# Kernel tuning notes

Hardware: AMD Instinct MI355X
Metric: run time of the kernel (lower is better)

Reference implementation:

```python
import jax, jax.numpy as jnp
import numpy as np

HEADS = 4
DIM_HEAD = 32


def setup_inputs() -> dict:
    key = jax.random.key(0)
    k1, k2, k3, k4 = jax.random.split(key, 4)
    dim = 64
    hidden = HEADS * DIM_HEAD  # 128
    x = jax.random.normal(k1, (1, dim, 16, 16, 16), jnp.float32)
    # Conv3d 1x1 kernels collapse to [out_ch, in_ch] matrices
    w_qkv = jax.random.normal(k2, (hidden * 3, dim), jnp.float32) * 0.05
    w_out = jax.random.normal(k3, (dim, hidden), jnp.float32) * 0.05
    b_out = jax.random.normal(k4, (dim,), jnp.float32) * 0.05
    return {"x": x, "w_qkv": w_qkv, "w_out": w_out, "b_out": b_out}


def reference(x, w_qkv, w_out, b_out):
    scale = DIM_HEAD ** -0.5
    b, c, dz, dy, dx = x.shape
    n = dz * dy * dx
    xf = x.reshape(b, c, n)  # flatten spatial dims
    # 1x1 Conv3d (no bias) == channel matmul: [b, 3*hidden, n]
    qkv = jnp.einsum('oc,bcn->bon', w_qkv, xf)
    q, k, v = jnp.split(qkv, 3, axis=1)  # each [b, hidden, n]
    def split_heads(t):
        return t.reshape(b, HEADS, DIM_HEAD, n)  # [b, h, d, n]
    q, k, v = split_heads(q), split_heads(k), split_heads(v)
    q = q * scale
    # sim[b,h,i,j] = sum_d q[b,h,d,i] k[b,h,d,j]
    sim = jnp.einsum('bhdi,bhdj->bhij', q, k)
    sim = sim - jax.lax.stop_gradient(jnp.max(sim, axis=-1, keepdims=True))
    attn = jax.nn.softmax(sim, axis=-1)
    # out[b,h,i,d] = sum_j attn[b,h,i,j] v[b,h,d,j]
    out = jnp.einsum('bhij,bhdj->bhid', attn, v)
    # 'b h (z y x) d -> b (h d) z y x'
    out = out.transpose(0, 1, 3, 2).reshape(b, HEADS * DIM_HEAD, n)
    # final 1x1 Conv3d with bias
    y = jnp.einsum('oc,bcn->bon', w_out, out) + b_out[None, :, None]
    return y.reshape(b, -1, dz, dy, dx)
```

## Files before the change

### kernel.cpp

```cpp
#include <hip/hip_runtime.h>


typedef _Float16 f16x8 __attribute__((ext_vector_type(8)));
typedef _Float16 f16x4 __attribute__((ext_vector_type(4)));
typedef _Float16 f16x2v __attribute__((ext_vector_type(2)));
typedef float f32x4 __attribute__((ext_vector_type(4)));

static __device__ inline f16x4 pack4(float a, float b, float c, float d) {
  f16x4 r;
  r.x = (_Float16)a; r.y = (_Float16)b; r.z = (_Float16)c; r.w = (_Float16)d;
  return r;
}
static __device__ inline f16x2v pack2(float a, float b) {
  f16x2v r;
  r.x = (_Float16)a; r.y = (_Float16)b;
  return r;
}

__global__ __launch_bounds__(256) void qkv_kernel(
    const float* __restrict__ x, const float* __restrict__ w,
    _Float16* __restrict__ qo, _Float16* __restrict__ ko, _Float16* __restrict__ vo)
{
  __shared__ __align__(16) float xs[64 * 68];
  __shared__ __align__(16) float wsb[32 * 68];
  const int t = threadIdx.x;
  const int n0 = blockIdx.x * 64;
  const int o0 = blockIdx.y * 32;
  #pragma unroll
  for (int i = 0; i < 4; ++i) {
    int ch = t + i * 256;
    int c = ch >> 4, p = ch & 15;
    *reinterpret_cast<float4*>(&xs[c * 68 + p * 4]) =
        *reinterpret_cast<const float4*>(&x[c * 4096 + n0 + p * 4]);
  }
  #pragma unroll
  for (int i = 0; i < 2; ++i) {
    int ch = t + i * 256;
    int o = ch >> 4, p = ch & 15;
    *reinterpret_cast<float4*>(&wsb[o * 68 + p * 4]) =
        *reinterpret_cast<const float4*>(&w[(o0 + o) * 64 + p * 4]);
  }
  __syncthreads();
  const int oL = (t >> 5) * 4;
  const int nL = (t & 31) * 2;
  float acc[4][2] = {};
  for (int c4 = 0; c4 < 64; c4 += 4) {
    float2 xa[4];
    #pragma unroll
    for (int k = 0; k < 4; ++k)
      xa[k] = *reinterpret_cast<const float2*>(&xs[(c4 + k) * 68 + nL]);
    #pragma unroll
    for (int i = 0; i < 4; ++i) {
      float4 wv = *reinterpret_cast<const float4*>(&wsb[(oL + i) * 68 + c4]);
      acc[i][0] += wv.x * xa[0].x + wv.y * xa[1].x + wv.z * xa[2].x + wv.w * xa[3].x;
      acc[i][1] += wv.x * xa[0].y + wv.y * xa[1].y + wv.z * xa[2].y + wv.w * xa[3].y;
    }
  }
  const float qs = 0.17677669529663689f * 1.4426950408889634f;
  if (o0 < 128) {
    int ho = o0 >> 5;
    #pragma unroll
    for (int j = 0; j < 2; ++j) {
      int n = n0 + nL + j;
      *reinterpret_cast<f16x4*>(&qo[(ho * 4096 + n) * 32 + oL]) =
          pack4(acc[0][j] * qs, acc[1][j] * qs, acc[2][j] * qs, acc[3][j] * qs);
    }
  } else if (o0 < 256) {
    int ho = (o0 - 128) >> 5;
    #pragma unroll
    for (int j = 0; j < 2; ++j) {
      int n = n0 + nL + j;
      *reinterpret_cast<f16x4*>(&ko[(ho * 4096 + n) * 32 + oL]) =
          pack4(acc[0][j], acc[1][j], acc[2][j], acc[3][j]);
    }
  } else {
    #pragma unroll
    for (int i = 0; i < 4; ++i) {
      *reinterpret_cast<f16x2v*>(&vo[(size_t)(o0 - 256 + oL + i) * 4096 + n0 + nL]) =
          pack2(acc[i][0], acc[i][1]);
    }
  }
}

__global__ __launch_bounds__(256, 4) void attn_kernel(
    const _Float16* __restrict__ qg, const _Float16* __restrict__ kg,
    const _Float16* __restrict__ vg, float* __restrict__ Opart,
    float* __restrict__ lpart, int jlen)
{
  __shared__ __align__(16) _Float16 Ks[2][64 * 40];
  __shared__ __align__(16) _Float16 Vs[2][32 * 72];
  const int t = threadIdx.x;
  const int ck = blockIdx.x;
  const int qt = blockIdx.y;
  const int h  = blockIdx.z;
  const int w = t >> 6;
  const int lane = t & 63;
  const int m = lane & 15;
  const int quad = lane >> 4;
  const int qw = qt * 128 + w * 32;

  f16x8 aq[2];
  #pragma unroll
  for (int g = 0; g < 2; ++g)
    aq[g] = *reinterpret_cast<const f16x8*>(
        &qg[(h * 4096 + qw + g * 16 + m) * 32 + quad * 8]);

  f32x4 acc[2][2];
  #pragma unroll
  for (int g = 0; g < 2; ++g) {
    acc[g][0] = f32x4{0.f, 0.f, 0.f, 0.f};
    acc[g][1] = f32x4{0.f, 0.f, 0.f, 0.f};
  }
  float ls[2] = {0.f, 0.f};

  const int jbeg = ck * jlen;
  const int kr = t >> 2, ksg = t & 3;
  const int vr = t >> 3, vsg = t & 7;
  const _Float16* kgp = kg + (size_t)(h * 4096 + jbeg + kr) * 32 + ksg * 8;
  const _Float16* vgp = vg + (size_t)(h * 32 + vr) * 4096 + jbeg + vsg * 8;

  *reinterpret_cast<uint4*>(&Ks[0][kr * 40 + ksg * 8]) =
      *reinterpret_cast<const uint4*>(kgp);
  *reinterpret_cast<uint4*>(&Vs[0][vr * 72 + vsg * 8]) =
      *reinterpret_cast<const uint4*>(vgp);
  __syncthreads();

  for (int it = 0; it < jlen; it += 64) {
    const int buf = (it >> 6) & 1;
    if (it + 64 < jlen) {
      *reinterpret_cast<uint4*>(&Ks[buf ^ 1][kr * 40 + ksg * 8]) =
          *reinterpret_cast<const uint4*>(kgp + (size_t)(it + 64) * 32);
      *reinterpret_cast<uint4*>(&Vs[buf ^ 1][vr * 72 + vsg * 8]) =
          *reinterpret_cast<const uint4*>(vgp + it + 64);
    }
    #pragma unroll
    for (int jt = 0; jt < 4; ++jt) {
      f16x8 kf = *reinterpret_cast<const f16x8*>(&Ks[buf][(jt * 16 + m) * 40 + quad * 8]);
      f16x4 vf0 = *reinterpret_cast<const f16x4*>(&Vs[buf][m * 72 + jt * 16 + quad * 4]);
      f16x4 vf1 = *reinterpret_cast<const f16x4*>(&Vs[buf][(16 + m) * 72 + jt * 16 + quad * 4]);
      f32x4 z = {0.f, 0.f, 0.f, 0.f};
      f32x4 sT[2];
      #pragma unroll
      for (int g = 0; g < 2; ++g)
        sT[g] = __builtin_amdgcn_mfma_f32_16x16x32_f16(kf, aq[g], z, 0, 0, 0);
      #pragma unroll
      for (int g = 0; g < 2; ++g) {
        float p0 = exp2f(sT[g][0]), p1 = exp2f(sT[g][1]);
        float p2 = exp2f(sT[g][2]), p3 = exp2f(sT[g][3]);
        ls[g] += (p0 + p1) + (p2 + p3);
        f16x4 p = pack4(p0, p1, p2, p3);
        acc[g][0] = __builtin_amdgcn_mfma_f32_16x16x16f16(p, vf0, acc[g][0], 0, 0, 0);
        acc[g][1] = __builtin_amdgcn_mfma_f32_16x16x16f16(p, vf1, acc[g][1], 0, 0, 0);
      }
    }
    __syncthreads();
  }

  #pragma unroll
  for (int g = 0; g < 2; ++g) {
    ls[g] += __shfl_xor(ls[g], 16);
    ls[g] += __shfl_xor(ls[g], 32);
  }
  const size_t cb = (size_t)(ck * 4 + h) * 4096;
  #pragma unroll
  for (int g = 0; g < 2; ++g) {
    #pragma unroll
    for (int dt = 0; dt < 2; ++dt) {
      #pragma unroll
      for (int r = 0; r < 4; ++r) {
        int q = qw + g * 16 + quad * 4 + r;
        Opart[(cb + q) * 32 + dt * 16 + m] = acc[g][dt][r];
      }
    }
  }
  if (quad == 0) {
    #pragma unroll
    for (int g = 0; g < 2; ++g)
      lpart[cb + qw + g * 16 + m] = ls[g];
  }
}

__global__ __launch_bounds__(256) void out_kernel(
    const float* __restrict__ Opart, const float* __restrict__ lpart,
    const float* __restrict__ wo, const float* __restrict__ bo,
    float* __restrict__ y)
{
  __shared__ __align__(16) float as[4 * 132];
  __shared__ __align__(16) float wsh[64 * 132];
  __shared__ float linv[16];
  const int t = threadIdx.x;
  const int nb = blockIdx.x * 4;
  if (t < 16) {
    int h = t >> 2, r = t & 3;
    float s = 0.f;
    #pragma unroll
    for (int ck = 0; ck < 8; ++ck)
      s += lpart[(size_t)(ck * 4 + h) * 4096 + nb + r];
    linv[t] = 1.f / s;
  }
  {
    int ch = t;
    #pragma unroll
    for (int i = 0; i < 8; ++i, ch += 256) {
      int r = ch >> 5, p = ch & 31;
      *reinterpret_cast<float4*>(&wsh[r * 132 + p * 4]) =
          *reinterpret_cast<const float4*>(&wo[r * 128 + p * 4]);
    }
  }
  __syncthreads();
  if (t < 128) {
    int r = t >> 5, p = t & 31;
    int h = p >> 3, d4 = (p & 7) * 4;
    float4 s = {0.f, 0.f, 0.f, 0.f};
    #pragma unroll
    for (int ck = 0; ck < 8; ++ck) {
      float4 o4 = *reinterpret_cast<const float4*>(
          &Opart[((size_t)(ck * 4 + h) * 4096 + nb + r) * 32 + d4]);
      s.x += o4.x; s.y += o4.y; s.z += o4.z; s.w += o4.w;
    }
    float inv = linv[h * 4 + r];
    s.x *= inv; s.y *= inv; s.z *= inv; s.w *= inv;
    *reinterpret_cast<float4*>(&as[r * 132 + p * 4]) = s;
  }
  __syncthreads();
  const int o = t >> 2;
  const int n = t & 3;
  float acc = 0.f;
  for (int c = 0; c < 128; c += 4) {
    float4 wv = *reinterpret_cast<const float4*>(&wsh[o * 132 + c]);
    float4 a  = *reinterpret_cast<const float4*>(&as[n * 132 + c]);
    acc += wv.x * a.x + wv.y * a.y + wv.z * a.z + wv.w * a.w;
  }
  y[(size_t)o * 4096 + nb + n] = acc + bo[o];
}

extern "C" void kernel_launch(void* const* d_in, const int* in_sizes, int n_in,
                              void* d_out, int out_size, void* d_ws, size_t ws_size,
                              hipStream_t stream) {
  (void)in_sizes; (void)n_in; (void)out_size; (void)ws_size;
  const float* x     = (const float*)d_in[0];
  const float* w_qkv = (const float*)d_in[1];
  const float* w_out = (const float*)d_in[2];
  const float* b_out = (const float*)d_in[3];
  float* y = (float*)d_out;
  _Float16* qb = (_Float16*)d_ws;
  _Float16* kb = qb + 524288;
  _Float16* vb = kb + 524288;
  float* Opart = (float*)(vb + 524288);
  float* lpart = Opart + 4194304;

  qkv_kernel<<<dim3(64, 12), 256, 0, stream>>>(x, w_qkv, qb, kb, vb);
  attn_kernel<<<dim3(8, 32, 4), 256, 0, stream>>>(qb, kb, vb, Opart, lpart, 4096 / 8);
  out_kernel<<<1024, 256, 0, stream>>>(Opart, lpart, w_out, b_out, y);
}
```

Measured before the change: 105.0 us.

## Double key splits and load each K/V chunk into LDS once

The attention kernel now splits the key dimension into 16 chunks of 256 instead of 8 chunks of 512, which doubles the grid to 2048 blocks. Each block loads its whole K/V chunk into shared memory up front, replacing the double-buffered 64-key pipeline, and drops the per-iteration barriers. The output kernel reduces 16 partial results instead of 8. The aim is more parallelism and less sync overhead. The cost is twice the partial-output traffic (Opart doubles to 32 MB of fp32) and a larger LDS footprint that may reduce occupancy.

```diff
diff --git a/kernel.cpp b/kernel.cpp
--- a/kernel.cpp
+++ b/kernel.cpp
@@ -85,19 +85,19 @@
 __global__ __launch_bounds__(256, 4) void attn_kernel(
     const _Float16* __restrict__ qg, const _Float16* __restrict__ kg,
     const _Float16* __restrict__ vg, float* __restrict__ Opart,
-    float* __restrict__ lpart, int jlen)
+    float* __restrict__ lpart)
 {
-  __shared__ __align__(16) _Float16 Ks[2][64 * 40];
-  __shared__ __align__(16) _Float16 Vs[2][32 * 72];
+  __shared__ __align__(16) _Float16 Ks[256 * 40];
+  __shared__ __align__(16) _Float16 Vs[32 * 264];
   const int t = threadIdx.x;
   const int ck = blockIdx.x;
   const int qt = blockIdx.y;
   const int h  = blockIdx.z;
-  const int w = t >> 6;
   const int lane = t & 63;
   const int m = lane & 15;
   const int quad = lane >> 4;
-  const int qw = qt * 128 + w * 32;
+  const int qw = qt * 128 + (t >> 6) * 32;
+  const int jbeg = ck * 256;
 
   f16x8 aq[2];
   #pragma unroll
@@ -105,6 +105,22 @@
     aq[g] = *reinterpret_cast<const f16x8*>(
         &qg[(h * 4096 + qw + g * 16 + m) * 32 + quad * 8]);
 
+  #pragma unroll
+  for (int i = 0; i < 4; ++i) {
+    int c = t + i * 256;
+    int r = c >> 2, sg = c & 3;
+    *reinterpret_cast<uint4*>(&Ks[r * 40 + sg * 8]) =
+        *reinterpret_cast<const uint4*>(&kg[(size_t)(h * 4096 + jbeg + r) * 32 + sg * 8]);
+  }
+  #pragma unroll
+  for (int i = 0; i < 4; ++i) {
+    int c = t + i * 256;
+    int r = c >> 5, sg = c & 31;
+    *reinterpret_cast<uint4*>(&Vs[r * 264 + sg * 8]) =
+        *reinterpret_cast<const uint4*>(&vg[(size_t)(h * 32 + r) * 4096 + jbeg + sg * 8]);
+  }
+  __syncthreads();
+
   f32x4 acc[2][2];
   #pragma unroll
   for (int g = 0; g < 2; ++g) {
@@ -113,31 +129,13 @@
   }
   float ls[2] = {0.f, 0.f};
 
-  const int jbeg = ck * jlen;
-  const int kr = t >> 2, ksg = t & 3;
-  const int vr = t >> 3, vsg = t & 7;
-  const _Float16* kgp = kg + (size_t)(h * 4096 + jbeg + kr) * 32 + ksg * 8;
-  const _Float16* vgp = vg + (size_t)(h * 32 + vr) * 4096 + jbeg + vsg * 8;
-
-  *reinterpret_cast<uint4*>(&Ks[0][kr * 40 + ksg * 8]) =
-      *reinterpret_cast<const uint4*>(kgp);
-  *reinterpret_cast<uint4*>(&Vs[0][vr * 72 + vsg * 8]) =
-      *reinterpret_cast<const uint4*>(vgp);
-  __syncthreads();
-
-  for (int it = 0; it < jlen; it += 64) {
-    const int buf = (it >> 6) & 1;
-    if (it + 64 < jlen) {
-      *reinterpret_cast<uint4*>(&Ks[buf ^ 1][kr * 40 + ksg * 8]) =
-          *reinterpret_cast<const uint4*>(kgp + (size_t)(it + 64) * 32);
-      *reinterpret_cast<uint4*>(&Vs[buf ^ 1][vr * 72 + vsg * 8]) =
-          *reinterpret_cast<const uint4*>(vgp + it + 64);
-    }
+  for (int it = 0; it < 256; it += 64) {
     #pragma unroll
     for (int jt = 0; jt < 4; ++jt) {
-      f16x8 kf = *reinterpret_cast<const f16x8*>(&Ks[buf][(jt * 16 + m) * 40 + quad * 8]);
-      f16x4 vf0 = *reinterpret_cast<const f16x4*>(&Vs[buf][m * 72 + jt * 16 + quad * 4]);
-      f16x4 vf1 = *reinterpret_cast<const f16x4*>(&Vs[buf][(16 + m) * 72 + jt * 16 + quad * 4]);
+      const int j0 = it + jt * 16;
+      f16x8 kf  = *reinterpret_cast<const f16x8*>(&Ks[(j0 + m) * 40 + quad * 8]);
+      f16x4 vf0 = *reinterpret_cast<const f16x4*>(&Vs[m * 264 + j0 + quad * 4]);
+      f16x4 vf1 = *reinterpret_cast<const f16x4*>(&Vs[(16 + m) * 264 + j0 + quad * 4]);
       f32x4 z = {0.f, 0.f, 0.f, 0.f};
       f32x4 sT[2];
       #pragma unroll
@@ -153,7 +151,6 @@
         acc[g][1] = __builtin_amdgcn_mfma_f32_16x16x16f16(p, vf1, acc[g][1], 0, 0, 0);
       }
     }
-    __syncthreads();
   }
 
   #pragma unroll
@@ -194,7 +191,7 @@
     int h = t >> 2, r = t & 3;
     float s = 0.f;
     #pragma unroll
-    for (int ck = 0; ck < 8; ++ck)
+    for (int ck = 0; ck < 16; ++ck)
       s += lpart[(size_t)(ck * 4 + h) * 4096 + nb + r];
     linv[t] = 1.f / s;
   }
@@ -213,7 +210,7 @@
     int h = p >> 3, d4 = (p & 7) * 4;
     float4 s = {0.f, 0.f, 0.f, 0.f};
     #pragma unroll
-    for (int ck = 0; ck < 8; ++ck) {
+    for (int ck = 0; ck < 16; ++ck) {
       float4 o4 = *reinterpret_cast<const float4*>(
           &Opart[((size_t)(ck * 4 + h) * 4096 + nb + r) * 32 + d4]);
       s.x += o4.x; s.y += o4.y; s.z += o4.z; s.w += o4.w;
@@ -247,9 +244,9 @@
   _Float16* kb = qb + 524288;
   _Float16* vb = kb + 524288;
   float* Opart = (float*)(vb + 524288);
-  float* lpart = Opart + 4194304;
+  float* lpart = Opart + 8388608;
 
   qkv_kernel<<<dim3(64, 12), 256, 0, stream>>>(x, w_qkv, qb, kb, vb);
-  attn_kernel<<<dim3(8, 32, 4), 256, 0, stream>>>(qb, kb, vb, Opart, lpart, 4096 / 8);
+  attn_kernel<<<dim3(16, 32, 4), 256, 0, stream>>>(qb, kb, vb, Opart, lpart);
   out_kernel<<<1024, 256, 0, stream>>>(Opart, lpart, w_out, b_out, y);
 }
```

Measured after the change: 105.4 us. About the same (+0.4%).
